# Kernel optimization log

Measured on AMD Instinct MI355X. Metric: run time of the kernel, lower is better.

The kernel has to match this reference:

```python
import jax, jax.numpy as jnp
import numpy as np

B, S, D = 4, 2048, 768
H, DH = 12, 64  # num heads, head dim


def setup_inputs() -> dict:
    key = jax.random.key(0)
    ks = jax.random.split(key, 4)
    scale = 0.02
    return {
        "hidden_states": jax.random.normal(ks[0], (B, S, D), dtype=jnp.float32),
        "attention_mask": jnp.zeros((B, 1, 1, S), dtype=jnp.float32),
        "Wq": jax.random.normal(ks[1], (D, D), dtype=jnp.float32) * scale,
        "bq": jnp.zeros((D,), dtype=jnp.float32),
        "Wk": jax.random.normal(ks[2], (D, D), dtype=jnp.float32) * scale,
        "bk": jnp.zeros((D,), dtype=jnp.float32),
        "Wv": jax.random.normal(ks[3], (D, D), dtype=jnp.float32) * scale,
        "bv": jnp.zeros((D,), dtype=jnp.float32),
    }


def _split_heads(x):
    # [B, S, D] -> [B, H, S, DH]
    b, s, _ = x.shape
    return x.reshape(b, s, H, DH).transpose(0, 2, 1, 3)


def reference(hidden_states, attention_mask, Wq, bq, Wk, bk, Wv, bv):
    q = _split_heads(hidden_states @ Wq.T + bq)
    k = _split_heads(hidden_states @ Wk.T + bk)
    v = _split_heads(hidden_states @ Wv.T + bv)
    # scores: [B, H, S, S]
    scores = jnp.einsum("bhqd,bhkd->bhqk", q, k) / jnp.sqrt(jnp.float32(DH))
    scores = scores + attention_mask
    probs = jax.nn.softmax(scores, axis=-1)
    # dropout prob = 0.0 (eval) -> identity
    ctx = jnp.einsum("bhqk,bhkd->bhqd", probs, v)
    ctx = ctx.transpose(0, 2, 1, 3).reshape(hidden_states.shape[0], hidden_states.shape[1], D)
    return ctx
```

## Files before the change

### kernel.cpp

```cpp
#include <hip/hip_runtime.h>

#define S_LEN 2048
#define DMODEL 768
#define NH 12
#define DHEAD 64
#define BATCH 4
#define MROWS (BATCH * S_LEN)
#define NQKV 2304
#define NQK 1536
#define LOG2E 1.4426950408889634f

using short8 = __attribute__((ext_vector_type(8))) short;
using f32x4  = __attribute__((ext_vector_type(4))) float;
using f32x16 = __attribute__((ext_vector_type(16))) float;

typedef const __attribute__((address_space(1))) void* gas_ptr;
typedef __attribute__((address_space(3))) void* las_ptr;

__device__ __forceinline__ void gl2lds16(const void* g, void* l) {
  __builtin_amdgcn_global_load_lds((gas_ptr)(unsigned long long)g,
                                   (las_ptr)(unsigned int)(unsigned long long)l,
                                   16, 0, 0);
}

__device__ __forceinline__ float fexp2(float x) {
  float r;
  asm("v_exp_f32 %0, %1" : "=v"(r) : "v"(x));
  return r;
}

__device__ __forceinline__ unsigned cvtpk(float lo, float hi) {
  unsigned r;
  asm("v_cvt_pk_bf16_f32 %0, %1, %2" : "=v"(r) : "v"(lo), "v"(hi));
  return r;
}

__device__ __forceinline__ void plswap(unsigned &a, unsigned &b) {
  asm("v_permlane32_swap_b32 %0, %1" : "+v"(a), "+v"(b));
}

__global__ __launch_bounds__(256) void prep_kernel(
    const float* __restrict__ hs, const float* __restrict__ Wq,
    const float* __restrict__ Wk, const float* __restrict__ Wv,
    const float* __restrict__ mask,
    unsigned short* __restrict__ Xb, unsigned short* __restrict__ Wall,
    float* __restrict__ mask2)
{
  const int NX = MROWS * DMODEL / 4;
  const int NW = DMODEL * DMODEL / 4;
  const int NM = (BATCH * S_LEN) / 4;
  int i = blockIdx.x * 256 + threadIdx.x;
  if (i < NX) {
    float4 f = ((const float4*)hs)[i];
    uint2 o = { cvtpk(f.x, f.y), cvtpk(f.z, f.w) };
    ((uint2*)Xb)[i] = o;
  } else if (i < NX + 3 * NW) {
    int j = i - NX;
    int sec = j / NW, r = j - sec * NW;
    const float* src = (sec == 0) ? Wq : (sec == 1) ? Wk : Wv;
    float4 f = ((const float4*)src)[r];
    uint2 o = { cvtpk(f.x, f.y), cvtpk(f.z, f.w) };
    ((uint2*)(Wall + (size_t)sec * DMODEL * DMODEL))[r] = o;
  } else if (i < NX + 3 * NW + NM) {
    int r = i - NX - 3 * NW;
    float4 m = ((const float4*)mask)[r];
    float4 o = { (m.x - 10.f) * LOG2E, (m.y - 10.f) * LOG2E,
                 (m.z - 10.f) * LOG2E, (m.w - 10.f) * LOG2E };
    ((float4*)mask2)[r] = o;
  }
}

__global__ __launch_bounds__(256) void qkv_gemm(
    const unsigned short* __restrict__ Xb,
    const unsigned short* __restrict__ Wall,
    const float* __restrict__ bq,
    const float* __restrict__ bk,
    const float* __restrict__ bv,
    unsigned short* __restrict__ QK,
    unsigned short* __restrict__ Vt)
{
  __shared__ __align__(16) short As[128][64];
  __shared__ __align__(16) short Bs[128][64];

  int gid = blockIdx.x;
  int x = gid & 7;
  int j = gid >> 3;
  int mloc = j / 18;
  int ntile = j - mloc * 18;
  int m0 = (x * 8 + mloc) * 128;
  int n0 = ntile * 128;

  int t = threadIdx.x;
  int w = t >> 6, lane = t & 63, lg = lane >> 4, lc = lane & 15;
  int wr = (w >> 1) * 64, wc = (w & 1) * 64;

  int srow = lane >> 3;
  int schunk = (lane & 7) ^ srow;

  f32x4 acc[4][4] = {};

  for (int k0 = 0; k0 < DMODEL; k0 += 64) {
    __syncthreads();
    for (int it = 0; it < 4; ++it) {
      int rb = w * 32 + it * 8;
      int r = rb + srow;
      gl2lds16(&Xb[(size_t)(m0 + r) * DMODEL + k0 + schunk * 8], &As[rb][0]);
      gl2lds16(&Wall[(size_t)(n0 + r) * DMODEL + k0 + schunk * 8], &Bs[rb][0]);
    }
    __syncthreads();
    for (int ks = 0; ks < 2; ++ks) {
      short8 a[4], b[4];
      for (int mt = 0; mt < 4; ++mt)
        a[mt] = *(const short8*)&As[wr + mt * 16 + lc][(((ks * 4 + lg) ^ (lc & 7))) * 8];
      for (int nt = 0; nt < 4; ++nt)
        b[nt] = *(const short8*)&Bs[wc + nt * 16 + lc][(((ks * 4 + lg) ^ (lc & 7))) * 8];
      for (int mt = 0; mt < 4; ++mt)
        for (int nt = 0; nt < 4; ++nt)
          acc[mt][nt] = __builtin_amdgcn_mfma_f32_16x16x32_bf16(a[mt], b[nt], acc[mt][nt], 0, 0, 0);
    }
  }

  if (n0 < 1536) {
    for (int nt = 0; nt < 4; ++nt) {
      int col = n0 + wc + nt * 16 + lc;
      float bb = (col < 768) ? bq[col] : bk[col - 768];
      float sc = (col < 768) ? (0.125f * LOG2E) : 1.0f;
      for (int mt = 0; mt < 4; ++mt) {
        int row = m0 + wr + mt * 16 + lg * 4;
        for (int i = 0; i < 4; ++i) {
          float v = (acc[mt][nt][i] + bb) * sc;
          QK[(size_t)(row + i) * NQK + col] = (unsigned short)cvtpk(v, v);
        }
      }
    }
  } else {
    int b2 = m0 >> 11;
    for (int nt = 0; nt < 4; ++nt) {
      int col = n0 + wc + nt * 16 + lc - 1536;
      int h2 = col >> 6, dd = col & 63;
      float bb = bv[col];
      size_t vbase = ((size_t)(b2 * NH + h2) * DHEAD + dd) * S_LEN;
      for (int mt = 0; mt < 4; ++mt) {
        int row = m0 + wr + mt * 16 + lg * 4;
        int s = row & (S_LEN - 1);
        float v0 = acc[mt][nt][0] + bb;
        float v1 = acc[mt][nt][1] + bb;
        float v2 = acc[mt][nt][2] + bb;
        float v3 = acc[mt][nt][3] + bb;
        uint2 d2 = { cvtpk(v0, v1), cvtpk(v2, v3) };
        *(uint2*)&Vt[vbase + s] = d2;
      }
    }
  }
}

__global__ __launch_bounds__(256, 4) void flash_attn(
    const unsigned short* __restrict__ QK,
    const unsigned short* __restrict__ Vt,
    const float* __restrict__ mask2,
    float* __restrict__ out)
{
  int gid = blockIdx.x;
  int x = gid & 7;
  int j = gid >> 3;
  int gloc = j >> 4;
  int qt = j & 15;
  int g = gloc * 8 + x;
  int h = g % NH;
  int b = g / NH;

  __shared__ __align__(16) short Ks[2][64][64];
  __shared__ __align__(16) short Vts[2][64][64];

  int t = threadIdx.x, w = t >> 6, lane = t & 63;
  int m31 = lane & 31, hf = lane >> 5;
  int q0 = qt * 128;
  int srow = lane >> 3;
  int schunk = (lane & 7) ^ srow;

  short8 qf[4];
  {
    size_t qrow = (size_t)(b * S_LEN + q0 + w * 32 + m31) * NQK + h * DHEAD;
#pragma unroll
    for (int kk = 0; kk < 4; ++kk)
      qf[kk] = *(const short8*)&QK[qrow + kk * 16 + hf * 8];
  }

  float lsum = 0.f;
  f32x16 o[2] = {};
  size_t vtbase = (size_t)((b * NH + h) * DHEAD) * S_LEN;
  size_t kbase0 = (size_t)(b * S_LEN) * NQK + 768 + h * DHEAD;
  const float* mrow = mask2 + (size_t)b * S_LEN;

#pragma unroll
  for (int it = 0; it < 2; ++it) {
    int rb = w * 16 + it * 8;
    int r = rb + srow;
    gl2lds16(&QK[kbase0 + (size_t)r * NQK + schunk * 8], &Ks[0][rb][0]);
    gl2lds16(&Vt[vtbase + (size_t)r * S_LEN + schunk * 8], &Vts[0][rb][0]);
  }

  int buf = 0;
  for (int kt = 0; kt < S_LEN / 64; ++kt) {
    int k0 = kt * 64;
    __syncthreads();

    {
      int ktn = (kt + 1 < S_LEN / 64) ? (kt + 1) : kt;
      int k0n = ktn * 64;
#pragma unroll
      for (int it = 0; it < 2; ++it) {
        int rb = w * 16 + it * 8;
        int r = rb + srow;
        gl2lds16(&QK[kbase0 + (size_t)(k0n + r) * NQK + schunk * 8], &Ks[buf ^ 1][rb][0]);
        gl2lds16(&Vt[vtbase + (size_t)r * S_LEN + k0n + schunk * 8], &Vts[buf ^ 1][rb][0]);
      }
    }

    f32x16 s[2] = {};
    __builtin_amdgcn_s_setprio(1);
#pragma unroll
    for (int kk = 0; kk < 4; ++kk)
#pragma unroll
      for (int mt = 0; mt < 2; ++mt) {
        int r = mt * 32 + m31;
        short8 ak = *(const short8*)&Ks[buf][r][((kk * 2 + hf) ^ (r & 7)) * 8];
        s[mt] = __builtin_amdgcn_mfma_f32_32x32x16_bf16(ak, qf[kk], s[mt], 0, 0, 0);
      }
    __builtin_amdgcn_s_setprio(0);

    unsigned pw[2][4][2];
#pragma unroll
    for (int mt = 0; mt < 2; ++mt)
#pragma unroll
      for (int gg = 0; gg < 4; ++gg) {
        float4 mv = *(const float4*)&mrow[k0 + mt * 32 + gg * 8 + hf * 4];
        float p0 = fexp2(s[mt][gg * 4 + 0] + mv.x);
        float p1 = fexp2(s[mt][gg * 4 + 1] + mv.y);
        float p2 = fexp2(s[mt][gg * 4 + 2] + mv.z);
        float p3 = fexp2(s[mt][gg * 4 + 3] + mv.w);
        lsum += (p0 + p1) + (p2 + p3);
        pw[mt][gg][0] = cvtpk(p0, p1);
        pw[mt][gg][1] = cvtpk(p2, p3);
      }

#pragma unroll
    for (int mt = 0; mt < 2; ++mt)
#pragma unroll
      for (int kk2 = 0; kk2 < 2; ++kk2) {
        unsigned a0 = pw[mt][2 * kk2][0], b0 = pw[mt][2 * kk2 + 1][0];
        unsigned a1 = pw[mt][2 * kk2][1], b1 = pw[mt][2 * kk2 + 1][1];
        plswap(a0, b0);
        plswap(a1, b1);
        union { unsigned u[4]; short8 v; } fr;
        fr.u[0] = a0; fr.u[1] = a1; fr.u[2] = b0; fr.u[3] = b1;
        int kk = mt * 2 + kk2;
        __builtin_amdgcn_s_setprio(1);
#pragma unroll
        for (int nt = 0; nt < 2; ++nt) {
          int r = nt * 32 + m31;
          short8 bvv = *(const short8*)&Vts[buf][r][((kk * 2 + hf) ^ (r & 7)) * 8];
          o[nt] = __builtin_amdgcn_mfma_f32_32x32x16_bf16(fr.v, bvv, o[nt], 0, 0, 0);
        }
        __builtin_amdgcn_s_setprio(0);
      }

    buf ^= 1;
  }

  lsum += __shfl_xor(lsum, 32, 64);
  float inv = 1.0f / lsum;
  float lv[16];
#pragma unroll
  for (int r = 0; r < 16; ++r)
    lv[r] = __shfl(inv, (r & 3) + 8 * (r >> 2) + 4 * hf, 64);

  for (int nt = 0; nt < 2; ++nt)
    for (int r = 0; r < 16; ++r) {
      int qrow = (r & 3) + 8 * (r >> 2) + 4 * hf;
      int q = q0 + w * 32 + qrow;
      out[(size_t)(b * S_LEN + q) * DMODEL + h * DHEAD + nt * 32 + m31] = o[nt][r] * lv[r];
    }
}

extern "C" void kernel_launch(void* const* d_in, const int* in_sizes, int n_in,
                              void* d_out, int out_size, void* d_ws, size_t ws_size,
                              hipStream_t stream) {
  const float* hs   = (const float*)d_in[0];
  const float* mask = (const float*)d_in[1];
  const float* Wq   = (const float*)d_in[2];
  const float* bq   = (const float*)d_in[3];
  const float* Wk   = (const float*)d_in[4];
  const float* bk   = (const float*)d_in[5];
  const float* Wv   = (const float*)d_in[6];
  const float* bv   = (const float*)d_in[7];
  float* out = (float*)d_out;

  char* ws = (char*)d_ws;
  const size_t XB_BYTES   = (size_t)MROWS * DMODEL * 2;
  const size_t QK_BYTES   = (size_t)MROWS * NQK * 2;
  const size_t VT_BYTES   = (size_t)BATCH * NH * DHEAD * S_LEN * 2;
  const size_t WALL_BYTES = (size_t)NQKV * DMODEL * 2;
  unsigned short* Xb    = (unsigned short*)ws;
  unsigned short* QK    = (unsigned short*)(ws + XB_BYTES);
  unsigned short* Vtg   = (unsigned short*)(ws + XB_BYTES + QK_BYTES);
  unsigned short* Wall  = (unsigned short*)(ws + XB_BYTES + QK_BYTES + VT_BYTES);
  float*          mask2 = (float*)(ws + XB_BYTES + QK_BYTES + VT_BYTES + WALL_BYTES);

  const int NX = MROWS * DMODEL / 4;
  const int NW = DMODEL * DMODEL / 4;
  const int NM = (BATCH * S_LEN) / 4;
  int nprep = NX + 3 * NW + NM;
  prep_kernel<<<(nprep + 255) / 256, 256, 0, stream>>>(hs, Wq, Wk, Wv, mask, Xb, Wall, mask2);

  qkv_gemm<<<1152, 256, 0, stream>>>(Xb, Wall, bq, bk, bv, QK, Vtg);

  flash_attn<<<768, 256, 0, stream>>>(QK, Vtg, mask2, out);
}
```

Measured before the change: 220.3 us.

## Split attention key range across two blocks and add a combine kernel

The flash attention grid is doubled so that each query tile's 2048 keys are split into two halves, each handled by its own block. Each block writes unnormalized partial outputs and row sums to workspace. A new combine kernel then adds the two partials and divides by the summed row sums. The aim is to better fill the GPU's compute units with 1536 blocks instead of 768. The cost is extra global memory traffic for the fp32 partials and one more kernel launch, and it relies on both halves using the same softmax scaling, with no per-split running max. The split path is used only when the workspace is large enough.

```diff
diff --git a/kernel.cpp b/kernel.cpp
--- a/kernel.cpp
+++ b/kernel.cpp
@@ -158,16 +158,23 @@
     const unsigned short* __restrict__ QK,
     const unsigned short* __restrict__ Vt,
     const float* __restrict__ mask2,
-    float* __restrict__ out)
+    float* __restrict__ out,
+    float* __restrict__ opart,
+    float* __restrict__ lpart,
+    int NS)
 {
   int gid = blockIdx.x;
   int x = gid & 7;
   int j = gid >> 3;
+  int ks = (NS == 2) ? (j & 1) : 0;
+  if (NS == 2) j >>= 1;
   int gloc = j >> 4;
   int qt = j & 15;
   int g = gloc * 8 + x;
   int h = g % NH;
   int b = g / NH;
+  int kt0 = ks * (32 / NS);
+  int ktend = kt0 + 32 / NS;
 
   __shared__ __align__(16) short Ks[2][64][64];
   __shared__ __align__(16) short Vts[2][64][64];
@@ -196,17 +203,17 @@
   for (int it = 0; it < 2; ++it) {
     int rb = w * 16 + it * 8;
     int r = rb + srow;
-    gl2lds16(&QK[kbase0 + (size_t)r * NQK + schunk * 8], &Ks[0][rb][0]);
-    gl2lds16(&Vt[vtbase + (size_t)r * S_LEN + schunk * 8], &Vts[0][rb][0]);
+    gl2lds16(&QK[kbase0 + (size_t)(kt0 * 64 + r) * NQK + schunk * 8], &Ks[0][rb][0]);
+    gl2lds16(&Vt[vtbase + (size_t)r * S_LEN + kt0 * 64 + schunk * 8], &Vts[0][rb][0]);
   }
 
   int buf = 0;
-  for (int kt = 0; kt < S_LEN / 64; ++kt) {
+  for (int kt = kt0; kt < ktend; ++kt) {
     int k0 = kt * 64;
     __syncthreads();
 
     {
-      int ktn = (kt + 1 < S_LEN / 64) ? (kt + 1) : kt;
+      int ktn = (kt + 1 < ktend) ? (kt + 1) : kt;
       int k0n = ktn * 64;
 #pragma unroll
       for (int it = 0; it < 2; ++it) {
@@ -269,18 +276,54 @@
   }
 
   lsum += __shfl_xor(lsum, 32, 64);
-  float inv = 1.0f / lsum;
-  float lv[16];
-#pragma unroll
-  for (int r = 0; r < 16; ++r)
-    lv[r] = __shfl(inv, (r & 3) + 8 * (r >> 2) + 4 * hf, 64);
-
-  for (int nt = 0; nt < 2; ++nt)
-    for (int r = 0; r < 16; ++r) {
-      int qrow = (r & 3) + 8 * (r >> 2) + 4 * hf;
-      int q = q0 + w * 32 + qrow;
-      out[(size_t)(b * S_LEN + q) * DMODEL + h * DHEAD + nt * 32 + m31] = o[nt][r] * lv[r];
-    }
+
+  if (NS == 1) {
+    float inv = 1.0f / lsum;
+    float lv[16];
+#pragma unroll
+    for (int r = 0; r < 16; ++r)
+      lv[r] = __shfl(inv, (r & 3) + 8 * (r >> 2) + 4 * hf, 64);
+    for (int nt = 0; nt < 2; ++nt)
+      for (int r = 0; r < 16; ++r) {
+        int qrow = (r & 3) + 8 * (r >> 2) + 4 * hf;
+        int q = q0 + w * 32 + qrow;
+        out[(size_t)(b * S_LEN + q) * DMODEL + h * DHEAD + nt * 32 + m31] = o[nt][r] * lv[r];
+      }
+  } else {
+    float* op = opart + (size_t)ks * MROWS * DMODEL;
+    for (int nt = 0; nt < 2; ++nt)
+      for (int r = 0; r < 16; ++r) {
+        int qrow = (r & 3) + 8 * (r >> 2) + 4 * hf;
+        int q = q0 + w * 32 + qrow;
+        op[(size_t)(b * S_LEN + q) * DMODEL + h * DHEAD + nt * 32 + m31] = o[nt][r];
+      }
+    if (hf == 0) {
+      int q = q0 + w * 32 + m31;
+      lpart[((size_t)ks * BATCH * NH + (b * NH + h)) * S_LEN + q] = lsum;
+    }
+  }
+}
+
+__global__ __launch_bounds__(256) void combine_kernel(
+    const float* __restrict__ op,
+    const float* __restrict__ lp,
+    float* __restrict__ out)
+{
+  const size_t OPSZ = (size_t)MROWS * DMODEL;
+  const size_t LPSZ = (size_t)BATCH * NH * S_LEN;
+  int i = blockIdx.x * 256 + threadIdx.x;
+  int row = i / 192;
+  int cq = i - row * 192;
+  int h = cq >> 4;
+  int b = row >> 11, s = row & (S_LEN - 1);
+  size_t lidx = (size_t)(b * NH + h) * S_LEN + s;
+  float l = lp[lidx] + lp[LPSZ + lidx];
+  float inv = 1.0f / l;
+  f32x4 a = *(const f32x4*)&op[(size_t)i * 4];
+  f32x4 c = *(const f32x4*)&op[OPSZ + (size_t)i * 4];
+  f32x4 r = { (a[0] + c[0]) * inv, (a[1] + c[1]) * inv,
+              (a[2] + c[2]) * inv, (a[3] + c[3]) * inv };
+  *(f32x4*)&out[(size_t)i * 4] = r;
 }
 
 extern "C" void kernel_launch(void* const* d_in, const int* in_sizes, int n_in,
@@ -301,12 +344,21 @@
   const size_t QK_BYTES   = (size_t)MROWS * NQK * 2;
   const size_t VT_BYTES   = (size_t)BATCH * NH * DHEAD * S_LEN * 2;
   const size_t WALL_BYTES = (size_t)NQKV * DMODEL * 2;
+  const size_t M2_BYTES   = (size_t)BATCH * S_LEN * 4;
   unsigned short* Xb    = (unsigned short*)ws;
   unsigned short* QK    = (unsigned short*)(ws + XB_BYTES);
   unsigned short* Vtg   = (unsigned short*)(ws + XB_BYTES + QK_BYTES);
   unsigned short* Wall  = (unsigned short*)(ws + XB_BYTES + QK_BYTES + VT_BYTES);
   float*          mask2 = (float*)(ws + XB_BYTES + QK_BYTES + VT_BYTES + WALL_BYTES);
 
+  size_t base = XB_BYTES + QK_BYTES + VT_BYTES + WALL_BYTES + M2_BYTES;
+  base = (base + 255) & ~(size_t)255;
+  const size_t OP_BYTES = 2 * (size_t)MROWS * DMODEL * 4;
+  const size_t LP_BYTES = 2 * (size_t)BATCH * NH * S_LEN * 4;
+  int NS = (ws_size >= base + OP_BYTES + LP_BYTES) ? 2 : 1;
+  float* opart = (float*)(ws + base);
+  float* lpart = (float*)(ws + base + OP_BYTES);
+
   const int NX = MROWS * DMODEL / 4;
   const int NW = DMODEL * DMODEL / 4;
   const int NM = (BATCH * S_LEN) / 4;
@@ -315,5 +367,8 @@
 
   qkv_gemm<<<1152, 256, 0, stream>>>(Xb, Wall, bq, bk, bv, QK, Vtg);
 
-  flash_attn<<<768, 256, 0, stream>>>(QK, Vtg, mask2, out);
-}
+  flash_attn<<<NS == 2 ? 1536 : 768, 256, 0, stream>>>(QK, Vtg, mask2, out, opart, lpart, NS);
+
+  if (NS == 2)
+    combine_kernel<<<MROWS * DMODEL / 4 / 256, 256, 0, stream>>>(opart, lpart, out);
+}
```

After: 229.2 us. +4.1%, slower.
